# Performance work log

Measured on AMD Instinct MI355X. Metric: run time of the kernel, lower is better.

Reference implementation:

```python
import jax, jax.numpy as jnp
import numpy as np

N_NODES = 20000
N_EDGES = 320000
N_GRAPHS = 512
N_FEAT = 29
DIMS = [N_FEAT, 1024, 512, 256, 512, 1024]
EPS = 1e-5


def setup_inputs() -> dict:
    key = jax.random.key(0)
    ks = jax.random.split(key, 32)
    inp = {}
    inp["x"] = jax.random.normal(ks[0], (N_NODES, N_FEAT), dtype=jnp.float32)
    inp["edge_index"] = jax.random.randint(ks[1], (2, N_EDGES), 0, N_NODES, dtype=jnp.int64)
    inp["batch"] = jnp.sort(jax.random.randint(ks[2], (N_NODES,), 0, N_GRAPHS, dtype=jnp.int64))
    # 5 GCNConv layers: weight [in, out] + bias, plus BN gamma/beta
    for i in range(5):
        din, dout = DIMS[i], DIMS[i + 1]
        inp[f"W{i+1}"] = jax.random.normal(ks[3 + i], (din, dout), dtype=jnp.float32) * (1.0 / np.sqrt(din))
        inp[f"b{i+1}"] = jnp.zeros((dout,), dtype=jnp.float32)
        inp[f"g{i+1}"] = jnp.ones((dout,), dtype=jnp.float32)
        inp[f"be{i+1}"] = jnp.zeros((dout,), dtype=jnp.float32)
    # attention gate Linear(1024, 1)
    inp["Wg"] = jax.random.normal(ks[10], (1024, 1), dtype=jnp.float32) * 0.03
    inp["bg"] = jnp.zeros((1,), dtype=jnp.float32)
    # MLP head
    inp["Wf2"] = jax.random.normal(ks[11], (1024, 128), dtype=jnp.float32) * 0.03
    inp["bf2"] = jnp.zeros((128,), dtype=jnp.float32)
    inp["Wf3"] = jax.random.normal(ks[12], (128, 16), dtype=jnp.float32) * 0.25
    inp["bf3"] = jnp.zeros((16,), dtype=jnp.float32)
    inp["Wf4"] = jax.random.normal(ks[13], (16, 1), dtype=jnp.float32) * 0.25
    inp["bf4"] = jnp.zeros((1,), dtype=jnp.float32)
    return inp


def _gcn_conv(x, row, col, W, b):
    # PyG GCNConv: linear transform, then D^{-1/2}(A+I)D^{-1/2} aggregation, then bias.
    n = x.shape[0]
    xw = x @ W  # [N, dout]
    deg = jax.ops.segment_sum(jnp.ones_like(col, dtype=xw.dtype), col, num_segments=n)
    dinv = jnp.where(deg > 0, jax.lax.rsqrt(deg), 0.0)
    norm = dinv[row] * dinv[col]  # [E+N]
    out = jax.ops.segment_sum(xw[row] * norm[:, None], col, num_segments=n)
    return out + b


def _bn_train(x, gamma, beta):
    m = jnp.mean(x, axis=0)
    v = jnp.var(x, axis=0)  # biased, matches torch training normalization
    return gamma * (x - m) * jax.lax.rsqrt(v + EPS) + beta


def _global_attention(x, batch, Wg, bg, n_graphs):
    gate = (x @ Wg + bg)[:, 0]  # [N]
    gmax = jax.ops.segment_max(gate, batch, num_segments=n_graphs)
    e = jnp.exp(gate - gmax[batch])
    s = jax.ops.segment_sum(e, batch, num_segments=n_graphs)
    alpha = e / s[batch]
    return jax.ops.segment_sum(alpha[:, None] * x, batch, num_segments=n_graphs)


def reference(x, edge_index, batch,
              W1, b1, g1, be1, W2, b2, g2, be2, W3, b3, g3, be3,
              W4, b4, g4, be4, W5, b5, g5, be5,
              Wg, bg, Wf2, bf2, Wf3, bf3, Wf4, bf4):
    n = x.shape[0]
    sl = jnp.arange(n, dtype=edge_index.dtype)
    row = jnp.concatenate([edge_index[0], sl])  # with self-loops
    col = jnp.concatenate([edge_index[1], sl])
    h = x
    params = [(W1, b1, g1, be1), (W2, b2, g2, be2), (W3, b3, g3, be3),
              (W4, b4, g4, be4), (W5, b5, g5, be5)]
    for (W, b, g, be) in params:
        h = jax.nn.relu(_gcn_conv(h, row, col, W, b))
        h = _bn_train(h, g, be)
    p = _global_attention(h, batch, Wg, bg, N_GRAPHS)  # [G, 1024]
    p = jax.nn.relu(p @ Wf2 + bf2)
    p = jax.nn.relu(p @ Wf3 + bf3)
    return p @ Wf4 + bf4  # [G, 1]
```

## Files before the change

kernel.cpp:

```cpp
#include <hip/hip_runtime.h>

#define EPS_BN 1e-5f

constexpr int NN   = 20000;
constexpr int NE   = 320000;
constexpr int NTOT = NE + NN;
constexpr int NG   = 512;
constexpr int MPAD = 20480;
constexpr int NBLK = 79;

typedef _Float16 half8  __attribute__((ext_vector_type(8)));
typedef _Float16 half2v __attribute__((ext_vector_type(2)));
typedef float floatx4   __attribute__((ext_vector_type(4)));

__device__ __forceinline__ void gload_lds16(const void* g, void* l) {
  __builtin_amdgcn_global_load_lds(
      (const __attribute__((address_space(1))) void*)g,
      (__attribute__((address_space(3))) void*)l, 16, 0, 0);
}

__global__ void k_deg(const int* __restrict__ col, int* __restrict__ deg,
                      const int* __restrict__ batch, int* __restrict__ gcnt) {
  int e = blockIdx.x * blockDim.x + threadIdx.x;
  if (e >= NTOT) return;
  int c = (e < NE) ? col[e] : (e - NE);
  atomicAdd(&deg[c], 1);
  if (e < NN) atomicAdd(&gcnt[batch[e]], 1);
}

__global__ __launch_bounds__(256) void k_pre1(const int* __restrict__ deg,
                                              float* __restrict__ dinvv,
                                              int* __restrict__ psum) {
  __shared__ int ws[4];
  int t = threadIdx.x, lane = t & 63, wv = t >> 6;
  int idx = blockIdx.x * 256 + t;
  int d = (idx < NN) ? deg[idx] : 0;
  if (idx < NN) dinvv[idx] = rsqrtf((float)d);
  int s = d;
  for (int o = 1; o < 64; o <<= 1) { int u = __shfl_up(s, o, 64); if (lane >= o) s += u; }
  if (lane == 63) ws[wv] = s;
  __syncthreads();
  if (t == 0) psum[blockIdx.x] = ws[0] + ws[1] + ws[2] + ws[3];
}

__global__ __launch_bounds__(256) void k_pre2(const int* __restrict__ psum,
                                              int* __restrict__ pbase,
                                              const int* __restrict__ gcnt,
                                              int* __restrict__ goff) {
  __shared__ int ws[8];
  int t = threadIdx.x, lane = t & 63, wv = t >> 6;
  int v = (t < NBLK) ? psum[t] : 0;
  int inc = v;
  for (int o = 1; o < 64; o <<= 1) { int u = __shfl_up(inc, o, 64); if (lane >= o) inc += u; }
  if (lane == 63) ws[wv] = inc;
  __syncthreads();
  int base = 0;
  for (int w = 0; w < wv; ++w) base += ws[w];
  int excl = base + inc - v;
  if (t < NBLK) pbase[t] = excl;
  if (t == NBLK - 1) pbase[NBLK] = excl + v;
  __syncthreads();
  int a0 = gcnt[2 * t], a1 = gcnt[2 * t + 1];
  int p = a0 + a1;
  int incp = p;
  for (int o = 1; o < 64; o <<= 1) { int u = __shfl_up(incp, o, 64); if (lane >= o) incp += u; }
  if (lane == 63) ws[4 + wv] = incp;
  __syncthreads();
  int gb = 0;
  for (int w = 0; w < wv; ++w) gb += ws[4 + w];
  int exclp = gb + incp - p;
  goff[2 * t]     = exclp;
  goff[2 * t + 1] = exclp + a0;
  if (t == 255) goff[NG] = exclp + p;
}

__global__ __launch_bounds__(256) void k_pre3(const int* __restrict__ deg,
                                              const int* __restrict__ pbase,
                                              int* __restrict__ indptr,
                                              int* __restrict__ cursor) {
  __shared__ int ws[4];
  int t = threadIdx.x, lane = t & 63, wv = t >> 6;
  int idx = blockIdx.x * 256 + t;
  int d = (idx < NN) ? deg[idx] : 0;
  int inc = d;
  for (int o = 1; o < 64; o <<= 1) { int u = __shfl_up(inc, o, 64); if (lane >= o) inc += u; }
  if (lane == 63) ws[wv] = inc;
  __syncthreads();
  int base = pbase[blockIdx.x];
  for (int w = 0; w < wv; ++w) base += ws[w];
  int excl = base + inc - d;
  if (idx < NN) { indptr[idx] = excl; cursor[idx] = excl; }
  if (idx == NN - 1) indptr[NN] = excl + d;
}

__global__ void k_fill(const int* __restrict__ row, const int* __restrict__ col,
                       const float* __restrict__ dinv, int* __restrict__ cursor,
                       int2* __restrict__ csw, float* __restrict__ rsum) {
  int e = blockIdx.x * blockDim.x + threadIdx.x;
  if (e >= NTOT) return;
  int r, c;
  if (e < NE) { r = row[e]; c = col[e]; } else { r = c = e - NE; }
  float wv = dinv[r] * dinv[c];
  int pos = atomicAdd(&cursor[c], 1);
  int2 m; m.x = r; m.y = __builtin_bit_cast(int, wv);
  csw[pos] = m;
  atomicAdd(&rsum[c], wv);
}

__global__ void k_wconv3(const float* __restrict__ W0, const float* __restrict__ W3,
                         const float* __restrict__ W4,
                         _Float16* __restrict__ T0, _Float16* __restrict__ T3,
                         _Float16* __restrict__ T4) {
  int idx = blockIdx.x * blockDim.x + threadIdx.x;
  if (idx < 32768) {
    int n = idx >> 5, k = idx & 31;
    T0[idx] = (_Float16)((k < 29) ? W0[(size_t)k * 1024 + n] : 0.f);
  } else if (idx < 32768 + 131072) {
    int j = idx - 32768;
    int n = j >> 8, k = j & 255;
    T3[j] = (_Float16)W3[(size_t)k * 512 + n];
  } else if (idx < 32768 + 131072 + 524288) {
    int j = idx - 163840;
    int n = j >> 9, k = j & 511;
    T4[j] = (_Float16)W4[(size_t)k * 1024 + n];
  }
}

__global__ __launch_bounds__(256) void k_wfold(const float* __restrict__ W, int K, int N,
                                               const float* __restrict__ sums,
                                               const float* __restrict__ gamma,
                                               const float* __restrict__ beta,
                                               _Float16* __restrict__ T,
                                               float* __restrict__ c) {
  __shared__ float red[256];
  int n = blockIdx.x, tid = threadIdx.x;
  const float inv_n = 1.f / NN;
  float csum = 0.f;
  for (int k = tid; k < K; k += 256) {
    float mean = sums[k] * inv_n;
    float var  = sums[K + k] * inv_n - mean * mean;
    float sc   = gamma[k] * rsqrtf(var + EPS_BN);
    float sh   = beta[k] - mean * sc;
    float wv   = W[(size_t)k * N + n];
    T[(size_t)n * K + k] = (_Float16)(sc * wv);
    csum += sh * wv;
  }
  red[tid] = csum;
  __syncthreads();
  for (int o = 128; o > 0; o >>= 1) {
    if (tid < o) red[tid] += red[tid + o];
    __syncthreads();
  }
  if (tid == 0) c[n] = red[0];
}

#define AGG_CH 128
__global__ __launch_bounds__(128) void k_agg29(
    const float* __restrict__ X,
    const int* __restrict__ indptr, const int2* __restrict__ csw,
    _Float16* __restrict__ Y) {
  __shared__ int   s_src[AGG_CH];
  __shared__ float s_w[AGG_CH];
  __shared__ float red[128];
  int node = blockIdx.x;
  int tid  = threadIdx.x;
  int sub  = tid / 29;
  int feat = tid - sub * 29;
  bool act = tid < 116;
  int beg = indptr[node], end = indptr[node + 1];
  float acc = 0.f;
  for (int e0 = beg; e0 < end; e0 += AGG_CH) {
    int c = min(AGG_CH, end - e0);
    if (tid < c) {
      int2 m = csw[e0 + tid];
      s_src[tid] = m.x;
      s_w[tid]   = __builtin_bit_cast(float, m.y);
    }
    __syncthreads();
    if (act) {
      for (int j = 0; j < c; j += 4) {
        int jj = j + sub;
        if (jj < c) acc += s_w[jj] * X[(size_t)s_src[jj] * 29 + feat];
      }
    }
    __syncthreads();
  }
  red[tid] = acc;
  __syncthreads();
  if (tid < 32) {
    float v = 0.f;
    if (tid < 29) v = red[tid] + red[29 + tid] + red[58 + tid] + red[87 + tid];
    Y[(size_t)node * 32 + tid] = (_Float16)v;
  }
}

template<int MODE>
__global__ __launch_bounds__(256) void k_aggv(
    const _Float16* __restrict__ X, _Float16* __restrict__ Y,
    const int* __restrict__ indptr, const int2* __restrict__ csw,
    const float* __restrict__ rowsum,
    const float* __restrict__ p0, const float* __restrict__ p1,
    const float* __restrict__ p2)
{
  constexpr int F = 512;
  int wave = threadIdx.x >> 6;
  int lane = threadIdx.x & 63;
  int node = blockIdx.x * 4 + wave;
  int beg = indptr[node], end = indptr[node + 1];
  float acc[8];
  #pragma unroll
  for (int i = 0; i < 8; ++i) acc[i] = 0.f;
  const unsigned* Xl = (const unsigned*)X + lane * 4;

  auto body = [&](int e) {
    int2 m = csw[e];
    float we = __builtin_bit_cast(float, m.y);
    uint4 d = *(const uint4*)(Xl + (size_t)m.x * (F / 2));
    unsigned uu[4] = {d.x, d.y, d.z, d.w};
    #pragma unroll
    for (int i = 0; i < 4; ++i) {
      half2v h = __builtin_bit_cast(half2v, uu[i]);
      acc[2 * i]     = fmaf(we, (float)h[0], acc[2 * i]);
      acc[2 * i + 1] = fmaf(we, (float)h[1], acc[2 * i + 1]);
    }
  };
  int e = beg;
  for (; e + 8 <= end; e += 8) {
    body(e); body(e + 1); body(e + 2); body(e + 3);
    body(e + 4); body(e + 5); body(e + 6); body(e + 7);
  }
  for (; e < end; ++e) body(e);

  float s_n = rowsum[node];
  size_t ob = (size_t)node * F + lane * 8;
  _Float16 outv[8];
  #pragma unroll
  for (int i = 0; i < 8; ++i) {
    int f = lane * 8 + i;
    float v;
    if constexpr (MODE == 0) {
      v = fmaxf(acc[i] + s_n * p0[f] + p1[f], 0.f);
    } else {
      const float inv_n = 1.f / NN;
      float mean = p0[f] * inv_n;
      float var  = p0[F + f] * inv_n - mean * mean;
      float sc   = p1[f] * rsqrtf(var + EPS_BN);
      float sh   = p2[f] - mean * sc;
      v = sc * acc[i] + s_n * sh;
    }
    outv[i] = (_Float16)v;
  }
  *(uint4*)(Y + ob) = *(const uint4*)outv;
}

template<int MODE>
__global__ __launch_bounds__(256) void k_aggp(
    const _Float16* __restrict__ X, _Float16* __restrict__ Y,
    const int* __restrict__ indptr, const int2* __restrict__ csw,
    const float* __restrict__ rowsum,
    const float* __restrict__ p0, const float* __restrict__ p1,
    const float* __restrict__ p2)
{
  constexpr int F = 256;
  int wave = threadIdx.x >> 6;
  int lane = threadIdx.x & 63;
  int half = lane >> 5;
  int l32  = lane & 31;
  int node = blockIdx.x * 8 + wave * 2 + half;
  int beg = indptr[node], end = indptr[node + 1];
  int len = end - beg;
  int len0 = __shfl(len, 0, 64);
  int len1 = __shfl(len, 32, 64);
  int maxlen = max(len0, len1);

  float acc[8];
  #pragma unroll
  for (int i = 0; i < 8; ++i) acc[i] = 0.f;
  const unsigned* Xl = (const unsigned*)X + l32 * 4;

  auto body = [&](int t) {
    int e = beg + min(t, len - 1);
    int2 m = csw[e];
    float we = (t < len) ? __builtin_bit_cast(float, m.y) : 0.f;
    uint4 d = *(const uint4*)(Xl + (size_t)m.x * (F / 2));
    unsigned uu[4] = {d.x, d.y, d.z, d.w};
    #pragma unroll
    for (int i = 0; i < 4; ++i) {
      half2v h = __builtin_bit_cast(half2v, uu[i]);
      acc[2 * i]     = fmaf(we, (float)h[0], acc[2 * i]);
      acc[2 * i + 1] = fmaf(we, (float)h[1], acc[2 * i + 1]);
    }
  };
  int t = 0;
  for (; t + 4 <= maxlen; t += 4) { body(t); body(t + 1); body(t + 2); body(t + 3); }
  for (; t < maxlen; ++t) body(t);

  float s_n = rowsum[node];
  size_t ob = (size_t)node * F + l32 * 8;
  _Float16 outv[8];
  #pragma unroll
  for (int i = 0; i < 8; ++i) {
    int f = l32 * 8 + i;
    float v;
    if constexpr (MODE == 0) {
      v = fmaxf(acc[i] + s_n * p0[f] + p1[f], 0.f);
    } else {
      const float inv_n = 1.f / NN;
      float mean = p0[f] * inv_n;
      float var  = p0[F + f] * inv_n - mean * mean;
      float sc   = p1[f] * rsqrtf(var + EPS_BN);
      float sh   = p2[f] - mean * sc;
      v = sc * acc[i] + s_n * sh;
    }
    outv[i] = (_Float16)v;
  }
  *(uint4*)(Y + ob) = *(const uint4*)outv;
}

template<int BK>
__global__ __launch_bounds__(256) void k_gemm16(
    const _Float16* __restrict__ A, const _Float16* __restrict__ B,
    const float* __restrict__ bias,
    _Float16* __restrict__ Ch,
    float* __restrict__ stats,
    int N, int K, int do_relu, int nbx)
{
  __shared__ __align__(16) union UU {
    struct { _Float16 a[128 * BK]; _Float16 b[128 * BK]; } ab;
    _Float16 c[128 * 136];
  } u;
  __shared__ float sred[256];

  const int tid  = threadIdx.x;
  const int wave = tid >> 6;
  const int lane = tid & 63;

  int lin = blockIdx.x;
  int xcd = lin & 7, seq = lin >> 3;
  int bx = seq % nbx, grp = seq / nbx;
  int by = xcd + 8 * grp;
  const int row0 = by * 128;
  const int col0 = bx * 128;

  const int q  = lane >> 4;
  const int mm = lane & 15;
  const int wm = wave >> 1;
  const int wn = wave & 1;

  sred[tid] = 0.f;

  constexpr int NREP = (BK == 32) ? 2 : 4;
  constexpr int RPW  = (BK == 32) ? 16 : 8;
  const _Float16* pA[NREP];
  const _Float16* pB[NREP];
  _Float16* dstA[NREP];
  _Float16* dstB[NREP];
  {
    int rl = (BK == 32) ? (lane >> 2) : (lane >> 3);
    int cp = (BK == 32) ? (lane & 3) : (lane & 7);
    #pragma unroll
    for (int rep = 0; rep < NREP; ++rep) {
      int trow = wave * 32 + rep * RPW;
      int s = (BK == 32) ? ((lane >> 3) & 3) : ((rep & 1) * 4 + (rl >> 1));
      int csrc = cp ^ s;
      pA[rep] = A + (size_t)(row0 + trow + rl) * K + csrc * 8;
      pB[rep] = B + (size_t)(col0 + trow + rl) * K + csrc * 8;
      dstA[rep] = u.ab.a + trow * BK;
      dstB[rep] = u.ab.b + trow * BK;
    }
  }

  const int sR = (BK == 32) ? ((mm >> 1) & 3) : (mm >> 1);
  int rdA[4], rdB[4];
  #pragma unroll
  for (int i = 0; i < 4; ++i) {
    rdA[i] = (wm * 64 + i * 16 + mm) * BK;
    rdB[i] = (wn * 64 + i * 16 + mm) * BK;
  }

  floatx4 acc[4][4];
  #pragma unroll
  for (int i = 0; i < 4; ++i)
    #pragma unroll
    for (int j = 0; j < 4; ++j) acc[i][j] = floatx4{0.f, 0.f, 0.f, 0.f};

  for (int k0 = 0; k0 < K; k0 += BK) {
    #pragma unroll
    for (int rep = 0; rep < NREP; ++rep) {
      gload_lds16(pA[rep], dstA[rep]);
      gload_lds16(pB[rep], dstB[rep]);
      pA[rep] += BK; pB[rep] += BK;
    }
    __syncthreads();

    #pragma unroll
    for (int kk = 0; kk < BK / 32; ++kk) {
      int pos = ((q + 4 * kk) ^ sR) * 8;
      half8 av[4];
      #pragma unroll
      for (int i = 0; i < 4; ++i) av[i] = *(const half8*)&u.ab.a[rdA[i] + pos];
      #pragma unroll
      for (int j = 0; j < 4; ++j) {
        half8 bv = *(const half8*)&u.ab.b[rdB[j] + pos];
        #pragma unroll
        for (int i = 0; i < 4; ++i)
          acc[i][j] = __builtin_amdgcn_mfma_f32_16x16x32_f16(av[i], bv, acc[i][j], 0, 0, 0);
      }
    }
    __syncthreads();
  }

  float sloc[4]  = {0.f, 0.f, 0.f, 0.f};
  float s2loc[4] = {0.f, 0.f, 0.f, 0.f};
  #pragma unroll
  for (int j = 0; j < 4; ++j) {
    int cl = wn * 64 + j * 16 + mm;
    float bv = bias ? bias[col0 + cl] : 0.f;
    #pragma unroll
    for (int i = 0; i < 4; ++i) {
      #pragma unroll
      for (int r = 0; r < 4; ++r) {
        int rl = wm * 64 + i * 16 + q * 4 + r;
        float v = acc[i][j][r] + bv;
        if (do_relu) v = fmaxf(v, 0.f);
        u.c[rl * 136 + cl] = (_Float16)v;
        if (row0 + rl < NN) { sloc[j] += v; s2loc[j] += v * v; }
      }
    }
  }

  if (stats) {
    #pragma unroll
    for (int j = 0; j < 4; ++j) {
      float a = sloc[j], b2 = s2loc[j];
      a  += __shfl_xor(a, 16, 64);  a  += __shfl_xor(a, 32, 64);
      b2 += __shfl_xor(b2, 16, 64); b2 += __shfl_xor(b2, 32, 64);
      if (q == 0) {
        int cl = wn * 64 + j * 16 + mm;
        atomicAdd(&sred[cl], a);
        atomicAdd(&sred[128 + cl], b2);
      }
    }
  }
  __syncthreads();

  #pragma unroll
  for (int pass = 0; pass < 8; ++pass) {
    int cidx = tid + pass * 256;
    int r = cidx >> 4, kc = cidx & 15;
    int rr = row0 + r;
    if (rr < NN) {
      uint4 d = *(const uint4*)&u.c[r * 136 + kc * 8];
      *(uint4*)&Ch[(size_t)rr * N + col0 + kc * 8] = d;
    }
  }

  if (stats && tid < 128) {
    atomicAdd(&stats[col0 + tid], sred[tid]);
    atomicAdd(&stats[N + col0 + tid], sred[128 + tid]);
  }
}

__global__ __launch_bounds__(256) void k_stats16(const _Float16* __restrict__ X, int F,
                                                 float* __restrict__ sums) {
  int tid = threadIdx.x;
  int npf = F >> 8;
  float s[2] = {0.f, 0.f}, s2[2] = {0.f, 0.f};
  for (int r = blockIdx.x; r < NN; r += gridDim.x) {
    #pragma unroll
    for (int i = 0; i < 2; ++i) {
      if (i < npf) {
        float v = (float)X[(size_t)r * F + tid + i * 256];
        s[i] += v; s2[i] += v * v;
      }
    }
  }
  #pragma unroll
  for (int i = 0; i < 2; ++i) {
    if (i < npf) {
      atomicAdd(&sums[tid + i * 256], s[i]);
      atomicAdd(&sums[F + tid + i * 256], s2[i]);
    }
  }
}

__global__ __launch_bounds__(256) void k_gate2(const _Float16* __restrict__ X,
                                               const float* __restrict__ sums,
                                               const float* __restrict__ g5,
                                               const float* __restrict__ be5,
                                               const float* __restrict__ Wg,
                                               const float* __restrict__ bg,
                                               float* __restrict__ gate) {
  __shared__ float red[512];
  int n = blockIdx.x, tid = threadIdx.x;
  int f = tid * 4;
  const float inv_n = 1.f / NN;
  uint2 u = *(const uint2*)(X + (size_t)n * 1024 + f);
  half2v h0 = __builtin_bit_cast(half2v, u.x);
  half2v h1 = __builtin_bit_cast(half2v, u.y);
  float xv[4] = {(float)h0[0], (float)h0[1], (float)h1[0], (float)h1[1]};
  float s = 0.f, t = 0.f;
  #pragma unroll
  for (int i = 0; i < 4; ++i) {
    int ff = f + i;
    float mean = sums[ff] * inv_n;
    float var  = sums[1024 + ff] * inv_n - mean * mean;
    float sc   = g5[ff] * rsqrtf(var + EPS_BN);
    float sh   = be5[ff] - mean * sc;
    float wg   = Wg[ff];
    s += xv[i] * (sc * wg);
    t += sh * wg;
  }
  red[tid] = s;
  red[256 + tid] = t;
  __syncthreads();
  for (int o = 128; o > 0; o >>= 1) {
    if (tid < o) { red[tid] += red[tid + o]; red[256 + tid] += red[256 + tid + o]; }
    __syncthreads();
  }
  if (tid == 0) gate[n] = red[0] + red[256] + bg[0];
}

__global__ __launch_bounds__(64) void k_segred(const float* __restrict__ gate,
                                               const int* __restrict__ goff,
                                               float* __restrict__ gmax,
                                               float* __restrict__ gsum) {
  int g = blockIdx.x, tid = threadIdx.x;
  int beg = goff[g], end = goff[g + 1];
  float m = -3.4e38f;
  for (int n = beg + tid; n < end; n += 64) m = fmaxf(m, gate[n]);
  for (int o = 32; o > 0; o >>= 1) m = fmaxf(m, __shfl_down(m, o, 64));
  m = __shfl(m, 0, 64);
  float s = 0.f;
  for (int n = beg + tid; n < end; n += 64) s += expf(gate[n] - m);
  for (int o = 32; o > 0; o >>= 1) s += __shfl_down(s, o, 64);
  if (tid == 0) { gmax[g] = m; gsum[g] = s; }
}

__global__ __launch_bounds__(256) void k_pool2(const _Float16* __restrict__ X,
                                               const float* __restrict__ gate,
                                               const int* __restrict__ goff,
                                               const float* __restrict__ gmax,
                                               const float* __restrict__ gsum,
                                               const float* __restrict__ sums,
                                               const float* __restrict__ g5,
                                               const float* __restrict__ be5,
                                               float* __restrict__ pooled) {
  int g = blockIdx.x, tid = threadIdx.x;
  int beg = goff[g], end = goff[g + 1];
  int f = tid * 4;
  const float inv_n = 1.f / NN;
  float acc[4] = {0.f, 0.f, 0.f, 0.f};
  bool nonempty = end > beg;
  if (nonempty) {
    float m = gmax[g], inv = 1.f / gsum[g];
    for (int n = beg; n < end; ++n) {
      float a = expf(gate[n] - m) * inv;
      uint2 u = *(const uint2*)(X + (size_t)n * 1024 + f);
      half2v h0 = __builtin_bit_cast(half2v, u.x);
      half2v h1 = __builtin_bit_cast(half2v, u.y);
      acc[0] += a * (float)h0[0];
      acc[1] += a * (float)h0[1];
      acc[2] += a * (float)h1[0];
      acc[3] += a * (float)h1[1];
    }
  }
  #pragma unroll
  for (int i = 0; i < 4; ++i) {
    int ff = f + i;
    float mean = sums[ff] * inv_n;
    float var  = sums[1024 + ff] * inv_n - mean * mean;
    float sc   = g5[ff] * rsqrtf(var + EPS_BN);
    float sh   = be5[ff] - mean * sc;
    float v = nonempty ? (acc[i] * sc + sh) : 0.f;
    pooled[(size_t)g * 1024 + ff] = v;
  }
}

__global__ __launch_bounds__(128) void k_head(const float* __restrict__ pooled,
                                              const float* __restrict__ Wf2, const float* __restrict__ bf2,
                                              const float* __restrict__ Wf3, const float* __restrict__ bf3,
                                              const float* __restrict__ Wf4, const float* __restrict__ bf4,
                                              float* __restrict__ out) {
  __shared__ float sp[1024];
  __shared__ float sp2[128];
  __shared__ float sp3[16];
  int g = blockIdx.x, tid = threadIdx.x;
  #pragma unroll
  for (int i = 0; i < 8; ++i) sp[tid + i * 128] = pooled[(size_t)g * 1024 + tid + i * 128];
  __syncthreads();
  float s = bf2[tid];
  for (int k = 0; k < 1024; ++k) s += sp[k] * Wf2[k * 128 + tid];
  sp2[tid] = fmaxf(s, 0.f);
  __syncthreads();
  if (tid < 16) {
    float t = bf3[tid];
    for (int k = 0; k < 128; ++k) t += sp2[k] * Wf3[k * 16 + tid];
    sp3[tid] = fmaxf(t, 0.f);
  }
  __syncthreads();
  if (tid == 0) {
    float t = bf4[0];
    for (int k = 0; k < 16; ++k) t += sp3[k] * Wf4[k];
    out[g] = t;
  }
}

extern "C" void kernel_launch(void* const* d_in, const int* in_sizes, int n_in,
                              void* d_out, int out_size, void* d_ws, size_t ws_size,
                              hipStream_t stream) {
  const float* x     = (const float*)d_in[0];
  const int*   ei    = (const int*)d_in[1];
  const int*   batch = (const int*)d_in[2];
  const float* W[5]; const float* b[5]; const float* g[5]; const float* be[5];
  for (int l = 0; l < 5; ++l) {
    W[l]  = (const float*)d_in[3 + 4 * l];
    b[l]  = (const float*)d_in[4 + 4 * l];
    g[l]  = (const float*)d_in[5 + 4 * l];
    be[l] = (const float*)d_in[6 + 4 * l];
  }
  const float* Wg  = (const float*)d_in[23];
  const float* bg  = (const float*)d_in[24];
  const float* Wf2 = (const float*)d_in[25];
  const float* bf2 = (const float*)d_in[26];
  const float* Wf3 = (const float*)d_in[27];
  const float* bf3 = (const float*)d_in[28];
  const float* Wf4 = (const float*)d_in[29];
  const float* bf4 = (const float*)d_in[30];
  float* out = (float*)d_out;

  const int* row = ei;
  const int* col = ei + NE;

  char* base = (char*)d_ws;
  size_t off = 0;
  auto alloc = [&](size_t bytes) -> char* {
    char* p = base + off;
    off = (off + bytes + 255) & ~(size_t)255;
    return p;
  };
  _Float16*  AH  = (_Float16*)alloc((size_t)MPAD * 1024 * 2);
  _Float16*  ASM = (_Float16*)alloc((size_t)MPAD * 32 * 2);
  _Float16*  BF  = (_Float16*)alloc((size_t)NN * 512 * 2);
  _Float16*  BF2 = (_Float16*)alloc((size_t)NN * 512 * 2);
  _Float16*  H5  = (_Float16*)alloc((size_t)NN * 1024 * 2);
  const int wtsz[5] = {1024 * 32, 512 * 1024, 256 * 512, 512 * 256, 1024 * 512};
  _Float16* WT[5];
  for (int l = 0; l < 5; ++l) WT[l] = (_Float16*)alloc((size_t)wtsz[l] * 2);
  float* c2  = (float*)alloc(512 * 4);
  float* c3  = (float*)alloc(256 * 4);
  float* dinv    = (float*)alloc(NN * 4);
  int*   indptr  = (int*)alloc((NN + 1) * 4);
  int*   cursor  = (int*)alloc(NN * 4);
  int2*  csw     = (int2*)alloc((size_t)NTOT * 8);
  int*   psum    = (int*)alloc((NBLK + 1) * 4);
  int*   pbase   = (int*)alloc((NBLK + 1) * 4);
  int*   goff    = (int*)alloc((NG + 1) * 4);
  float* gate    = (float*)alloc(NN * 4);
  float* gmax    = (float*)alloc(NG * 4);
  float* gsum    = (float*)alloc(NG * 4);
  float* pooled  = (float*)alloc((size_t)NG * 1024 * 4);
  size_t znf = 6656 + NN + NG + NN;
  float* zbase = (float*)alloc(znf * 4);
  float* bns  = zbase;
  int*   deg  = (int*)(zbase + 6656);
  int*   gcnt = (int*)(zbase + 6656 + NN);
  float* rsum = zbase + 6656 + NN + NG;
  float* bns1 = bns;
  float* bns2 = bns + 2048;
  float* bns3 = bns + 3072;
  float* bns4 = bns + 3584;
  float* bns5 = bns + 4608;

  hipMemsetAsync(zbase, 0, znf * 4, stream);
  k_deg<<<(NTOT + 255) / 256, 256, 0, stream>>>(col, deg, batch, gcnt);
  k_pre1<<<NBLK, 256, 0, stream>>>(deg, dinv, psum);
  k_pre2<<<1, 256, 0, stream>>>(psum, pbase, gcnt, goff);
  k_pre3<<<NBLK, 256, 0, stream>>>(deg, pbase, indptr, cursor);
  k_fill<<<(NTOT + 255) / 256, 256, 0, stream>>>(row, col, dinv, cursor, csw, rsum);
  k_wconv3<<<2688, 256, 0, stream>>>(W[0], W[3], W[4], WT[0], WT[3], WT[4]);

  auto gemm = [&](const _Float16* Aop, int wl, const float* bias,
                  _Float16* Ch, float* stats, int Nn, int Kk, int relu) {
    int nbx = Nn / 128;
    if (Kk == 32)
      k_gemm16<32><<<nbx * 160, 256, 0, stream>>>(Aop, WT[wl], bias, Ch, stats, Nn, Kk, relu, nbx);
    else
      k_gemm16<64><<<nbx * 160, 256, 0, stream>>>(Aop, WT[wl], bias, Ch, stats, Nn, Kk, relu, nbx);
  };

  k_agg29<<<NN, 128, 0, stream>>>(x, indptr, csw, ASM);
  gemm(ASM, 0, b[0], AH, bns1, 1024, 32, 1);

  k_wfold<<<512, 256, 0, stream>>>(W[1], 1024, 512, bns1, g[0], be[0], WT[1], c2);
  gemm(AH, 1, nullptr, BF, nullptr, 512, 1024, 0);
  k_aggv<0><<<NN / 4, 256, 0, stream>>>(BF, AH, indptr, csw, rsum, c2, b[1], nullptr);
  k_stats16<<<512, 256, 0, stream>>>(AH, 512, bns2);

  k_wfold<<<256, 256, 0, stream>>>(W[2], 512, 256, bns2, g[1], be[1], WT[2], c3);
  gemm(AH, 2, nullptr, BF2, nullptr, 256, 512, 0);
  k_aggp<0><<<NN / 8, 256, 0, stream>>>(BF2, BF, indptr, csw, rsum, c3, b[2], nullptr);
  k_stats16<<<512, 256, 0, stream>>>(BF, 256, bns3);

  k_aggp<1><<<NN / 8, 256, 0, stream>>>(BF, AH, indptr, csw, rsum, bns3, g[2], be[2]);
  gemm(AH, 3, b[3], BF2, bns4, 512, 256, 1);

  k_aggv<1><<<NN / 4, 256, 0, stream>>>(BF2, AH, indptr, csw, rsum, bns4, g[3], be[3]);
  gemm(AH, 4, b[4], H5, bns5, 1024, 512, 1);

  k_gate2<<<NN, 256, 0, stream>>>(H5, bns5, g[4], be[4], Wg, bg, gate);
  k_segred<<<NG, 64, 0, stream>>>(gate, goff, gmax, gsum);
  k_pool2<<<NG, 256, 0, stream>>>(H5, gate, goff, gmax, gsum, bns5, g[4], be[4], pooled);

  k_head<<<NG, 128, 0, stream>>>(pooled, Wf2, bf2, Wf3, bf3, Wf4, bf4, out);
}
```

Baseline: 618.1 us.

## Pre-swizzle weights into MFMA fragment layout and fuse pooling with MLP head

Result: faster. 591.4 us (-4.3%).

```diff
diff --git a/kernel.cpp b/kernel.cpp
--- a/kernel.cpp
+++ b/kernel.cpp
@@ -107,22 +107,36 @@
   atomicAdd(&rsum[c], wv);
 }
 
+__device__ __forceinline__ size_t fragoff(int n, int k, int kb) {
+  return ((size_t)(n >> 4) * kb + (k >> 5)) * 512 + ((k >> 3) & 3) * 128 + (n & 15) * 8;
+}
+
 __global__ void k_wconv3(const float* __restrict__ W0, const float* __restrict__ W3,
                          const float* __restrict__ W4,
                          _Float16* __restrict__ T0, _Float16* __restrict__ T3,
                          _Float16* __restrict__ T4) {
-  int idx = blockIdx.x * blockDim.x + threadIdx.x;
-  if (idx < 32768) {
-    int n = idx >> 5, k = idx & 31;
-    T0[idx] = (_Float16)((k < 29) ? W0[(size_t)k * 1024 + n] : 0.f);
-  } else if (idx < 32768 + 131072) {
-    int j = idx - 32768;
-    int n = j >> 8, k = j & 255;
-    T3[j] = (_Float16)W3[(size_t)k * 512 + n];
-  } else if (idx < 32768 + 131072 + 524288) {
-    int j = idx - 163840;
-    int n = j >> 9, k = j & 511;
-    T4[j] = (_Float16)W4[(size_t)k * 1024 + n];
+  int c = blockIdx.x * blockDim.x + threadIdx.x;
+  _Float16 ov[8];
+  if (c < 4096) {
+    int n = c >> 2, k = (c & 3) * 8;
+    #pragma unroll
+    for (int i = 0; i < 8; ++i)
+      ov[i] = (_Float16)((k + i < 29) ? W0[(size_t)(k + i) * 1024 + n] : 0.f);
+    *(uint4*)&T0[fragoff(n, k, 1)] = *(const uint4*)ov;
+  } else if (c < 4096 + 16384) {
+    int c2 = c - 4096;
+    int n = c2 >> 5, k = (c2 & 31) * 8;
+    #pragma unroll
+    for (int i = 0; i < 8; ++i)
+      ov[i] = (_Float16)W3[(size_t)(k + i) * 512 + n];
+    *(uint4*)&T3[fragoff(n, k, 8)] = *(const uint4*)ov;
+  } else if (c < 4096 + 16384 + 65536) {
+    int c3 = c - 20480;
+    int n = c3 >> 6, k = (c3 & 63) * 8;
+    #pragma unroll
+    for (int i = 0; i < 8; ++i)
+      ov[i] = (_Float16)W4[(size_t)(k + i) * 1024 + n];
+    *(uint4*)&T4[fragoff(n, k, 16)] = *(const uint4*)ov;
   }
 }
 
@@ -134,16 +148,24 @@
                                                float* __restrict__ c) {
   __shared__ float red[256];
   int n = blockIdx.x, tid = threadIdx.x;
+  int kb = K >> 5;
   const float inv_n = 1.f / NN;
   float csum = 0.f;
-  for (int k = tid; k < K; k += 256) {
-    float mean = sums[k] * inv_n;
-    float var  = sums[K + k] * inv_n - mean * mean;
-    float sc   = gamma[k] * rsqrtf(var + EPS_BN);
-    float sh   = beta[k] - mean * sc;
-    float wv   = W[(size_t)k * N + n];
-    T[(size_t)n * K + k] = (_Float16)(sc * wv);
-    csum += sh * wv;
+  for (int kc = tid; kc < (K >> 3); kc += 256) {
+    int k = kc * 8;
+    _Float16 ov[8];
+    #pragma unroll
+    for (int i = 0; i < 8; ++i) {
+      int ki = k + i;
+      float mean = sums[ki] * inv_n;
+      float var  = sums[K + ki] * inv_n - mean * mean;
+      float sc   = gamma[ki] * rsqrtf(var + EPS_BN);
+      float sh   = beta[ki] - mean * sc;
+      float wv   = W[(size_t)ki * N + n];
+      ov[i] = (_Float16)(sc * wv);
+      csum += sh * wv;
+    }
+    *(uint4*)&T[fragoff(n, k, kb)] = *(const uint4*)ov;
   }
   red[tid] = csum;
   __syncthreads();
@@ -319,14 +341,14 @@
 
 template<int BK>
 __global__ __launch_bounds__(256) void k_gemm16(
-    const _Float16* __restrict__ A, const _Float16* __restrict__ B,
+    const _Float16* __restrict__ A, const _Float16* __restrict__ Bf,
     const float* __restrict__ bias,
     _Float16* __restrict__ Ch,
     float* __restrict__ stats,
     int N, int K, int do_relu, int nbx)
 {
   __shared__ __align__(16) union UU {
-    struct { _Float16 a[128 * BK]; _Float16 b[128 * BK]; } ab;
+    _Float16 a[128 * BK];
     _Float16 c[128 * 136];
   } u;
   __shared__ float sred[256];
@@ -352,9 +374,7 @@
   constexpr int NREP = (BK == 32) ? 2 : 4;
   constexpr int RPW  = (BK == 32) ? 16 : 8;
   const _Float16* pA[NREP];
-  const _Float16* pB[NREP];
   _Float16* dstA[NREP];
-  _Float16* dstB[NREP];
   {
     int rl = (BK == 32) ? (lane >> 2) : (lane >> 3);
     int cp = (BK == 32) ? (lane & 3) : (lane & 7);
@@ -364,19 +384,20 @@
       int s = (BK == 32) ? ((lane >> 3) & 3) : ((rep & 1) * 4 + (rl >> 1));
       int csrc = cp ^ s;
       pA[rep] = A + (size_t)(row0 + trow + rl) * K + csrc * 8;
-      pB[rep] = B + (size_t)(col0 + trow + rl) * K + csrc * 8;
-      dstA[rep] = u.ab.a + trow * BK;
-      dstB[rep] = u.ab.b + trow * BK;
+      dstA[rep] = u.a + trow * BK;
     }
   }
 
   const int sR = (BK == 32) ? ((mm >> 1) & 3) : (mm >> 1);
-  int rdA[4], rdB[4];
-  #pragma unroll
-  for (int i = 0; i < 4; ++i) {
-    rdA[i] = (wm * 64 + i * 16 + mm) * BK;
-    rdB[i] = (wn * 64 + i * 16 + mm) * BK;
-  }
+  int rdA[4];
+  #pragma unroll
+  for (int i = 0; i < 4; ++i) rdA[i] = (wm * 64 + i * 16 + mm) * BK;
+
+  const int kb = K >> 5;
+  const _Float16* pb[4];
+  #pragma unroll
+  for (int j = 0; j < 4; ++j)
+    pb[j] = Bf + (size_t)((col0 + wn * 64 + j * 16) >> 4) * kb * 512 + lane * 8;
 
   floatx4 acc[4][4];
   #pragma unroll
@@ -388,24 +409,24 @@
     #pragma unroll
     for (int rep = 0; rep < NREP; ++rep) {
       gload_lds16(pA[rep], dstA[rep]);
-      gload_lds16(pB[rep], dstB[rep]);
-      pA[rep] += BK; pB[rep] += BK;
+      pA[rep] += BK;
     }
     __syncthreads();
 
     #pragma unroll
     for (int kk = 0; kk < BK / 32; ++kk) {
+      half8 bv[4];
+      #pragma unroll
+      for (int j = 0; j < 4; ++j) { bv[j] = *(const half8*)pb[j]; pb[j] += 512; }
       int pos = ((q + 4 * kk) ^ sR) * 8;
       half8 av[4];
       #pragma unroll
-      for (int i = 0; i < 4; ++i) av[i] = *(const half8*)&u.ab.a[rdA[i] + pos];
+      for (int i = 0; i < 4; ++i) av[i] = *(const half8*)&u.a[rdA[i] + pos];
       #pragma unroll
-      for (int j = 0; j < 4; ++j) {
-        half8 bv = *(const half8*)&u.ab.b[rdB[j] + pos];
+      for (int j = 0; j < 4; ++j)
         #pragma unroll
         for (int i = 0; i < 4; ++i)
-          acc[i][j] = __builtin_amdgcn_mfma_f32_16x16x32_f16(av[i], bv, acc[i][j], 0, 0, 0);
-      }
+          acc[i][j] = __builtin_amdgcn_mfma_f32_16x16x32_f16(av[i], bv[j], acc[i][j], 0, 0, 0);
     }
     __syncthreads();
   }
@@ -521,39 +542,48 @@
   if (tid == 0) gate[n] = red[0] + red[256] + bg[0];
 }
 
-__global__ __launch_bounds__(64) void k_segred(const float* __restrict__ gate,
-                                               const int* __restrict__ goff,
-                                               float* __restrict__ gmax,
-                                               float* __restrict__ gsum) {
+__global__ __launch_bounds__(256) void k_poolhead(
+    const _Float16* __restrict__ X, const float* __restrict__ gate,
+    const int* __restrict__ goff,
+    const float* __restrict__ sums, const float* __restrict__ g5,
+    const float* __restrict__ be5,
+    const float* __restrict__ Wf2, const float* __restrict__ bf2,
+    const float* __restrict__ Wf3, const float* __restrict__ bf3,
+    const float* __restrict__ Wf4, const float* __restrict__ bf4,
+    float* __restrict__ out)
+{
+  __shared__ float red[256];
+  __shared__ float sp[1024];
+  __shared__ float sp2[128];
+  __shared__ float sp3[16];
   int g = blockIdx.x, tid = threadIdx.x;
   int beg = goff[g], end = goff[g + 1];
+  bool nonempty = end > beg;
+
   float m = -3.4e38f;
-  for (int n = beg + tid; n < end; n += 64) m = fmaxf(m, gate[n]);
-  for (int o = 32; o > 0; o >>= 1) m = fmaxf(m, __shfl_down(m, o, 64));
-  m = __shfl(m, 0, 64);
+  for (int n = beg + tid; n < end; n += 256) m = fmaxf(m, gate[n]);
+  red[tid] = m;
+  __syncthreads();
+  for (int o = 128; o > 0; o >>= 1) {
+    if (tid < o) red[tid] = fmaxf(red[tid], red[tid + o]);
+    __syncthreads();
+  }
+  m = red[0];
+  __syncthreads();
   float s = 0.f;
-  for (int n = beg + tid; n < end; n += 64) s += expf(gate[n] - m);
-  for (int o = 32; o > 0; o >>= 1) s += __shfl_down(s, o, 64);
-  if (tid == 0) { gmax[g] = m; gsum[g] = s; }
-}
-
-__global__ __launch_bounds__(256) void k_pool2(const _Float16* __restrict__ X,
-                                               const float* __restrict__ gate,
-                                               const int* __restrict__ goff,
-                                               const float* __restrict__ gmax,
-                                               const float* __restrict__ gsum,
-                                               const float* __restrict__ sums,
-                                               const float* __restrict__ g5,
-                                               const float* __restrict__ be5,
-                                               float* __restrict__ pooled) {
-  int g = blockIdx.x, tid = threadIdx.x;
-  int beg = goff[g], end = goff[g + 1];
+  for (int n = beg + tid; n < end; n += 256) s += expf(gate[n] - m);
+  red[tid] = s;
+  __syncthreads();
+  for (int o = 128; o > 0; o >>= 1) {
+    if (tid < o) red[tid] += red[tid + o];
+    __syncthreads();
+  }
+  float inv = nonempty ? (1.f / red[0]) : 0.f;
+
   int f = tid * 4;
   const float inv_n = 1.f / NN;
   float acc[4] = {0.f, 0.f, 0.f, 0.f};
-  bool nonempty = end > beg;
   if (nonempty) {
-    float m = gmax[g], inv = 1.f / gsum[g];
     for (int n = beg; n < end; ++n) {
       float a = expf(gate[n] - m) * inv;
       uint2 u = *(const uint2*)(X + (size_t)n * 1024 + f);
@@ -572,26 +602,15 @@
     float var  = sums[1024 + ff] * inv_n - mean * mean;
     float sc   = g5[ff] * rsqrtf(var + EPS_BN);
     float sh   = be5[ff] - mean * sc;
-    float v = nonempty ? (acc[i] * sc + sh) : 0.f;
-    pooled[(size_t)g * 1024 + ff] = v;
-  }
-}
-
-__global__ __launch_bounds__(128) void k_head(const float* __restrict__ pooled,
-                                              const float* __restrict__ Wf2, const float* __restrict__ bf2,
-                                              const float* __restrict__ Wf3, const float* __restrict__ bf3,
-                                              const float* __restrict__ Wf4, const float* __restrict__ bf4,
-                                              float* __restrict__ out) {
-  __shared__ float sp[1024];
-  __shared__ float sp2[128];
-  __shared__ float sp3[16];
-  int g = blockIdx.x, tid = threadIdx.x;
-  #pragma unroll
-  for (int i = 0; i < 8; ++i) sp[tid + i * 128] = pooled[(size_t)g * 1024 + tid + i * 128];
-  __syncthreads();
-  float s = bf2[tid];
-  for (int k = 0; k < 1024; ++k) s += sp[k] * Wf2[k * 128 + tid];
-  sp2[tid] = fmaxf(s, 0.f);
+    sp[ff] = nonempty ? (acc[i] * sc + sh) : 0.f;
+  }
+  __syncthreads();
+
+  if (tid < 128) {
+    float s2 = bf2[tid];
+    for (int k = 0; k < 1024; ++k) s2 += sp[k] * Wf2[k * 128 + tid];
+    sp2[tid] = fmaxf(s2, 0.f);
+  }
   __syncthreads();
   if (tid < 16) {
     float t = bf3[tid];
@@ -657,9 +676,6 @@
   int*   pbase   = (int*)alloc((NBLK + 1) * 4);
   int*   goff    = (int*)alloc((NG + 1) * 4);
   float* gate    = (float*)alloc(NN * 4);
-  float* gmax    = (float*)alloc(NG * 4);
-  float* gsum    = (float*)alloc(NG * 4);
-  float* pooled  = (float*)alloc((size_t)NG * 1024 * 4);
   size_t znf = 6656 + NN + NG + NN;
   float* zbase = (float*)alloc(znf * 4);
   float* bns  = zbase;
@@ -678,7 +694,7 @@
   k_pre2<<<1, 256, 0, stream>>>(psum, pbase, gcnt, goff);
   k_pre3<<<NBLK, 256, 0, stream>>>(deg, pbase, indptr, cursor);
   k_fill<<<(NTOT + 255) / 256, 256, 0, stream>>>(row, col, dinv, cursor, csw, rsum);
-  k_wconv3<<<2688, 256, 0, stream>>>(W[0], W[3], W[4], WT[0], WT[3], WT[4]);
+  k_wconv3<<<336, 256, 0, stream>>>(W[0], W[3], W[4], WT[0], WT[3], WT[4]);
 
   auto gemm = [&](const _Float16* Aop, int wl, const float* bias,
                   _Float16* Ch, float* stats, int Nn, int Kk, int relu) {
@@ -709,8 +725,6 @@
   gemm(AH, 4, b[4], H5, bns5, 1024, 512, 1);
 
   k_gate2<<<NN, 256, 0, stream>>>(H5, bns5, g[4], be[4], Wg, bg, gate);
-  k_segred<<<NG, 64, 0, stream>>>(gate, goff, gmax, gsum);
-  k_pool2<<<NG, 256, 0, stream>>>(H5, gate, goff, gmax, gsum, bns5, g[4], be[4], pooled);
-
-  k_head<<<NG, 128, 0, stream>>>(pooled, Wf2, bf2, Wf3, bf3, Wf4, bf4, out);
-}
+  k_poolhead<<<NG, 256, 0, stream>>>(H5, gate, goff, bns5, g[4], be[4],
+                                     Wf2, bf2, Wf3, bf3, Wf4, bf4, out);
+}
```
